# Optimization experiments

Hardware: AMD Instinct MI355X
Metric: run time of the kernel (lower is better)

Reference implementation:

```python
import jax, jax.numpy as jnp
import numpy as np

N = 20000      # nodes
E = 320000     # edges per relation
D = 128        # d_model
H = 2          # attention heads


def _gat(x, src, dst, W, al, ar, b):
    """DGL-style GATConv on a single relation (same src/dst node type).
    x: [N, in], W: [in, H*O], al/ar: [H, O], b: [H*O]. Returns [N, H, O]."""
    h, o = al.shape
    feat = (x @ W).reshape(N, h, o)                 # [N, H, O]
    el = jnp.sum(feat * al, axis=-1)                # [N, H]
    er = jnp.sum(feat * ar, axis=-1)                # [N, H]
    e = jax.nn.leaky_relu(el[src] + er[dst], 0.2)   # [E, H] per-edge logits
    m = jax.ops.segment_max(e, dst, num_segments=N)            # per-dst max
    ee = jnp.exp(e - m[dst])
    s = jax.ops.segment_sum(ee, dst, num_segments=N)
    alpha = ee / jnp.maximum(s[dst], 1e-9)          # edge softmax over incoming edges
    out = jax.ops.segment_sum(alpha[:, :, None] * feat[src], dst, num_segments=N)
    return out + b.reshape(1, h, o)


def setup_inputs() -> dict:
    key = jax.random.key(0)
    ks = jax.random.split(key, 24)
    d = {
        'x': jax.random.normal(ks[0], (N, D), jnp.float32),
        'src0': jax.random.randint(ks[1], (E,), 0, N, jnp.int32),
        'dst0': jax.random.randint(ks[2], (E,), 0, N, jnp.int32),
        'src1': jax.random.randint(ks[3], (E,), 0, N, jnp.int32),
        'dst1': jax.random.randint(ks[4], (E,), 0, N, jnp.int32),
    }
    sc = 0.1
    # layer 1: in=D, out per head=2D, heads=H
    d['W1_0'] = jax.random.normal(ks[5], (D, H * 2 * D), jnp.float32) * sc
    d['al1_0'] = jax.random.normal(ks[6], (H, 2 * D), jnp.float32) * sc
    d['ar1_0'] = jax.random.normal(ks[7], (H, 2 * D), jnp.float32) * sc
    d['b1_0'] = jnp.zeros((H * 2 * D,), jnp.float32)
    d['W1_1'] = jax.random.normal(ks[8], (D, H * 2 * D), jnp.float32) * sc
    d['al1_1'] = jax.random.normal(ks[9], (H, 2 * D), jnp.float32) * sc
    d['ar1_1'] = jax.random.normal(ks[10], (H, 2 * D), jnp.float32) * sc
    d['b1_1'] = jnp.zeros((H * 2 * D,), jnp.float32)
    # layer 2: in=2D, out per head=D, heads=H
    d['W2_0'] = jax.random.normal(ks[11], (2 * D, H * D), jnp.float32) * sc
    d['al2_0'] = jax.random.normal(ks[12], (H, D), jnp.float32) * sc
    d['ar2_0'] = jax.random.normal(ks[13], (H, D), jnp.float32) * sc
    d['b2_0'] = jnp.zeros((H * D,), jnp.float32)
    d['W2_1'] = jax.random.normal(ks[14], (2 * D, H * D), jnp.float32) * sc
    d['al2_1'] = jax.random.normal(ks[15], (H, D), jnp.float32) * sc
    d['ar2_1'] = jax.random.normal(ks[16], (H, D), jnp.float32) * sc
    d['b2_1'] = jnp.zeros((H * D,), jnp.float32)
    return d


def reference(x, src0, dst0, src1, dst1,
              W1_0, al1_0, ar1_0, b1_0, W1_1, al1_1, ar1_1, b1_1,
              W2_0, al2_0, ar2_0, b2_0, W2_1, al2_1, ar2_1, b2_1):
    # conv1: HeteroGraphConv sum over relations, then mean over heads, relu
    h1 = _gat(x, src0, dst0, W1_0, al1_0, ar1_0, b1_0) \
       + _gat(x, src1, dst1, W1_1, al1_1, ar1_1, b1_1)   # [N, H, 2D]
    h1 = jax.nn.relu(h1.mean(axis=1))                    # [N, 2D]; dropout is eval-mode identity
    # conv2: same structure, then mean over heads
    h2 = _gat(h1, src0, dst0, W2_0, al2_0, ar2_0, b2_0) \
       + _gat(h1, src1, dst1, W2_1, al2_1, ar2_1, b2_1)  # [N, H, D]
    return h2.mean(axis=1)                                # [N, D]
```

## Files before the change

kernel.cpp:

```cpp
#include <hip/hip_runtime.h>


#define NN 20000
#define NE 320000
#define LOG2E 1.44269504f

typedef unsigned short bf16_t;
typedef __attribute__((ext_vector_type(8))) short short8;
typedef __attribute__((ext_vector_type(4))) float f32x4;

__device__ __forceinline__ float bf2f(bf16_t u) {
    return __uint_as_float(((unsigned)u) << 16);
}
__device__ __forceinline__ bf16_t f2bf(float f) {
    unsigned x = __float_as_uint(f);
    unsigned r = (x + 0x7fffu + ((x >> 16) & 1u)) >> 16;
    return (bf16_t)r;
}
__device__ __forceinline__ unsigned pk2bf(float a, float b) {
    return (unsigned)f2bf(a) | ((unsigned)f2bf(b) << 16);
}
__device__ __forceinline__ float lrelu(float v) {
    return (v > 0.f) ? v : 0.2f * v;
}
__device__ __forceinline__ void load_x2(const void* x, int flag, int idx,
                                        float& v0, float& v1) {
    if (flag) {
        float2 f = ((const float2*)x)[idx];
        v0 = f.x; v1 = f.y;
    } else {
        unsigned pk = ((const unsigned*)x)[idx];
        v0 = bf2f((bf16_t)(pk & 0xffffu));
        v1 = bf2f((bf16_t)(pk >> 16));
    }
}

#define NTC 16
struct CzArgs {
    const void* src[NTC];
    bf16_t* dst[NTC];
    int n[NTC];
    int nblk[NTC + 1];
    int* zero_ptr;
    int zn;
    const unsigned* xsrc;
    int* flag_out;
};
__global__ void convzero_kernel(CzArgs a) {
    __shared__ int fl_s;
    int t = threadIdx.x;
    if (t < 64) {
        float mx = 0.f;
        for (int i = t; i < 256; i += 64) {
            float v = fabsf(bf2f((bf16_t)(a.xsrc[i] & 0xffffu)));
            v = (v <= 1e30f) ? v : 1e30f;
            mx = fmaxf(mx, v);
        }
        for (int off = 32; off > 0; off >>= 1) mx = fmaxf(mx, __shfl_xor(mx, off));
        if (t == 0) {
            int f = (mx > 1e6f) ? 1 : 0;
            fl_s = f;
            if (blockIdx.x == 0) *a.flag_out = f;
        }
    }
    __syncthreads();
    int flag = fl_s;
    int b = blockIdx.x;
    int ti = 0;
#pragma unroll 1
    for (; ti <= NTC; ++ti) {
        if (b < a.nblk[ti]) break;
        b -= a.nblk[ti];
    }
    int i = b * 256 + t;
    if (ti < NTC) {
        if (i < a.n[ti]) {
            if (flag) a.dst[ti][i] = f2bf(((const float*)a.src[ti])[i]);
            else      a.dst[ti][i] = ((const bf16_t*)a.src[ti])[i];
        }
    } else {
        if (i < a.zn) a.zero_ptr[i] = 0;
    }
}

struct PrepArgs {
    const bf16_t *W1[2], *W2[2];
    const bf16_t *al1[2], *ar1[2], *al2[2], *ar2[2];
    const bf16_t *b1[2], *b2[2];
    float *wal1, *war1;
    float *wal2, *war2;
    float *bc1, *bc2;
    bf16_t *Wc1f;
    bf16_t *Wzf;
};
__device__ __forceinline__ void prep_body(const PrepArgs& p, int bx, int tid) {
    if (bx < 4) {
        int t = bx * 256 + tid;
        int lr = t >> 9, rel = (t >> 8) & 1, h = (t >> 7) & 1, k = t & 127;
        const bf16_t* av = lr ? p.ar1[rel] : p.al1[rel];
        const bf16_t* W = p.W1[rel];
        float s = 0.f;
        for (int o = 0; o < 256; ++o)
            s += bf2f(W[k * 512 + h * 256 + o]) * bf2f(av[h * 256 + o]);
        (lr ? p.war1 : p.wal1)[(rel * 2 + h) * 128 + k] = s * LOG2E;
    } else if (bx < 12) {
        int t = (bx - 4) * 256 + tid;
        int lr = t >> 10, rel = (t >> 9) & 1, h = (t >> 8) & 1, k = t & 255;
        const bf16_t* av = lr ? p.ar2[rel] : p.al2[rel];
        const bf16_t* W = p.W2[rel];
        float s = 0.f;
        for (int o = 0; o < 128; ++o)
            s += bf2f(W[k * 256 + h * 128 + o]) * bf2f(av[h * 128 + o]);
        (lr ? p.war2 : p.wal2)[(rel * 2 + h) * 256 + k] = s * LOG2E;
    } else if (bx < 14) {
        int t = (bx - 12) * 256 + tid;
        if (t < 256) {
            p.bc1[t] = 0.5f * (bf2f(p.b1[0][t]) + bf2f(p.b1[0][256 + t]) +
                               bf2f(p.b1[1][t]) + bf2f(p.b1[1][256 + t]));
        } else if (t < 384) {
            int o = t - 256;
            p.bc2[o] = 0.5f * (bf2f(p.b2[0][o]) + bf2f(p.b2[0][128 + o]) +
                               bf2f(p.b2[1][o]) + bf2f(p.b2[1][128 + o]));
        }
    } else if (bx < 78) {
        int i = (bx - 14) * 256 + tid;
        int lane = i & 63;
        int t2 = i >> 6;
        int ct = t2 >> 4, ks = t2 & 15;
        int col = ct * 16 + (lane & 15);
        bf16_t* out = p.Wc1f + (size_t)i * 8;
#pragma unroll
        for (int j = 0; j < 8; ++j) {
            int r = ks * 32 + ((lane >> 4) << 3) + j;
            int rel = r >> 8, h = (r >> 7) & 1, kx = r & 127;
            out[j] = f2bf(0.5f * bf2f(p.W1[rel][kx * 512 + h * 256 + col]));
        }
    } else {
        int b = bx - 78;
        int rel = b >> 5;
        int i = (b & 31) * 256 + tid;
        int lane = i & 63;
        int t2 = i >> 6;
        int ct = t2 >> 3, ks = t2 & 7;
        int col = ct * 16 + (lane & 15);
        bf16_t* out = p.Wzf + (size_t)rel * 65536 + (size_t)i * 8;
#pragma unroll
        for (int j = 0; j < 8; ++j) {
            int r = ks * 32 + ((lane >> 4) << 3) + j;
            out[j] = f2bf(0.5f * bf2f(p.W2[rel][r * 256 + col]));
        }
    }
}

struct Csr2 {
    const int* src[2];
    const int* dst[2];
    int* cnt[2];
    int* offs[2];
    int* rank[2];
    int* srcc[2];
};
struct PhArgs { PrepArgs p; Csr2 c; };
__global__ void prep_hist_kernel(PhArgs a) {
    int bx = blockIdx.x;
    if (bx < 142) {
        prep_body(a.p, bx, threadIdx.x);
    } else {
        int b = bx - 142;
        int rel = b / 1250;
        int i = (b - rel * 1250) * 256 + threadIdx.x;
        if (i < NE)
            a.c.rank[rel][i] = atomicAdd(&a.c.cnt[rel][a.c.dst[rel][i]], 1);
    }
}

__global__ void scan2_kernel(Csr2 c, int n) {
    int rel = blockIdx.x;
    const int* cnt = c.cnt[rel];
    int* offs = c.offs[rel];
    __shared__ int sums[1024];
    int t = threadIdx.x;
    int chunk = (n + 1023) >> 10;
    int lo = t * chunk;
    int hi = min(lo + chunk, n);
    int s = 0;
    for (int i = lo; i < hi; ++i) s += cnt[i];
    sums[t] = s;
    __syncthreads();
    for (int off = 1; off < 1024; off <<= 1) {
        int v = (t >= off) ? sums[t - off] : 0;
        __syncthreads();
        sums[t] += v;
        __syncthreads();
    }
    int run = (t == 0) ? 0 : sums[t - 1];
    for (int i = lo; i < hi; ++i) { int v = cnt[i]; offs[i] = run; run += v; }
    if (t == 1023) offs[n] = sums[1023];
}

__global__ void scat_elr_kernel(Csr2 c, const void* __restrict__ x,
                                const int* __restrict__ flagp,
                                const float* __restrict__ wal1,
                                const float* __restrict__ war1,
                                float* __restrict__ el0, float* __restrict__ er0,
                                float* __restrict__ el1, float* __restrict__ er1) {
    __shared__ float wl[512], wr[512];
    int t = threadIdx.x;
    if (blockIdx.x < 5000) {
        wl[t] = wal1[t]; wl[t + 256] = wal1[t + 256];
        wr[t] = war1[t]; wr[t + 256] = war1[t + 256];
        __syncthreads();
        int fl = *flagp;
        int w = t >> 6, lane = t & 63;
        int node = blockIdx.x * 4 + w;
        float v0, v1;
        load_x2(x, fl, node * 64 + lane, v0, v1);
        float de[4], dr[4];
#pragma unroll
        for (int cch = 0; cch < 4; ++cch) {
            de[cch] = v0 * wl[cch * 128 + 2 * lane] + v1 * wl[cch * 128 + 2 * lane + 1];
            dr[cch] = v0 * wr[cch * 128 + 2 * lane] + v1 * wr[cch * 128 + 2 * lane + 1];
        }
#pragma unroll
        for (int off = 32; off > 0; off >>= 1) {
#pragma unroll
            for (int cch = 0; cch < 4; ++cch) {
                de[cch] += __shfl_xor(de[cch], off);
                dr[cch] += __shfl_xor(dr[cch], off);
            }
        }
        if (lane == 0) {
            el0[node * 2 + 0] = de[0]; el0[node * 2 + 1] = de[1];
            el1[node * 2 + 0] = de[2]; el1[node * 2 + 1] = de[3];
            er0[node * 2 + 0] = dr[0]; er0[node * 2 + 1] = dr[1];
            er1[node * 2 + 0] = dr[2]; er1[node * 2 + 1] = dr[3];
        }
    } else {
        int b = blockIdx.x - 5000;
        int rel = b / 313;
        int base = (b - rel * 313) * 1024 + t * 4;
        const int* dstp = c.dst[rel];
        const int* srcp = c.src[rel];
        const int* rkp  = c.rank[rel];
        const int* offp = c.offs[rel];
        int* sc = c.srcc[rel];
        if (base + 3 < NE) {
            int4 dv = *(const int4*)(dstp + base);
            int4 rv = *(const int4*)(rkp + base);
            int4 sv = *(const int4*)(srcp + base);
            sc[offp[dv.x] + rv.x] = sv.x;
            sc[offp[dv.y] + rv.y] = sv.y;
            sc[offp[dv.z] + rv.z] = sv.z;
            sc[offp[dv.w] + rv.w] = sv.w;
        } else {
            for (int k = 0; k < 4 && base + k < NE; ++k)
                sc[offp[dstp[base + k]] + rkp[base + k]] = srcp[base + k];
        }
    }
}

__device__ __forceinline__ void wave_softmax(
    const int* __restrict__ srcc, int beg, int deg,
    const float* __restrict__ el, float er_h0, float er_h1, int lane,
    int& sreg, float& a0, float& a1,
    float& m0, float& i0, float& m1, float& i1) {
    float mm0 = -1e30f, ss0 = 0.f, mm1 = -1e30f, ss1 = 0.f;
    float e0r = 0.f, e1r = 0.f;
    sreg = 0;
    for (int j = lane; j < deg; j += 64) {
        int s = srcc[beg + j];
        float2 ev = ((const float2*)el)[s];
        float e0 = lrelu(ev.x + er_h0);
        float e1 = lrelu(ev.y + er_h1);
        if (j < 64) { sreg = s; e0r = e0; e1r = e1; }
        float mn0 = fmaxf(mm0, e0);
        ss0 = ss0 * exp2f(mm0 - mn0) + exp2f(e0 - mn0);
        mm0 = mn0;
        float mn1 = fmaxf(mm1, e1);
        ss1 = ss1 * exp2f(mm1 - mn1) + exp2f(e1 - mn1);
        mm1 = mn1;
    }
#pragma unroll
    for (int off = 1; off < 64; off <<= 1) {
        float om = __shfl_xor(mm0, off), os = __shfl_xor(ss0, off);
        float mn = fmaxf(mm0, om);
        ss0 = ss0 * exp2f(mm0 - mn) + os * exp2f(om - mn);
        mm0 = mn;
        om = __shfl_xor(mm1, off); os = __shfl_xor(ss1, off);
        mn = fmaxf(mm1, om);
        ss1 = ss1 * exp2f(mm1 - mn) + os * exp2f(om - mn);
        mm1 = mn;
    }
    m0 = mm0; m1 = mm1;
    i0 = 1.f / fmaxf(ss0, 1e-9f);
    i1 = 1.f / fmaxf(ss1, 1e-9f);
    a0 = exp2f(e0r - m0) * i0;
    a1 = exp2f(e1r - m1) * i1;
}

__global__ void agg1_kernel(
    const int* __restrict__ offs0, const int* __restrict__ srcc0,
    const float* __restrict__ el0, const float* __restrict__ er0,
    const int* __restrict__ offs1, const int* __restrict__ srcc1,
    const float* __restrict__ el1, const float* __restrict__ er1,
    const void* __restrict__ x, const int* __restrict__ flagp,
    bf16_t* __restrict__ y1) {
    int t = threadIdx.x;
    int w = t >> 6, lane = t & 63;
    int slot = lane >> 5, m = lane & 31;
    int d = blockIdx.x * 2 + (w >> 1);
    int rel = w & 1;
    const int* offs = rel ? offs1 : offs0;
    const int* srcc = rel ? srcc1 : srcc0;
    const float* el = rel ? el1 : el0;
    const float* er = rel ? er1 : er0;
    int beg = offs[d], deg = offs[d + 1] - beg;
    float erh0 = er[d * 2], erh1 = er[d * 2 + 1];
    int fl = *flagp;

    int sr;
    float a0, a1, m0, i0, m1, i1;
    wave_softmax(srcc, beg, deg, el, erh0, erh1, lane, sr, a0, a1, m0, i0, m1, i1);

    auto xload = [&](int s, float v[4]) {
        if (fl) {
            float4 f = ((const float4*)x)[s * 32 + m];
            v[0] = f.x; v[1] = f.y; v[2] = f.z; v[3] = f.w;
        } else {
            uint2 pk = ((const uint2*)x)[s * 32 + m];
            v[0] = bf2f((bf16_t)(pk.x & 0xffffu));
            v[1] = bf2f((bf16_t)(pk.x >> 16));
            v[2] = bf2f((bf16_t)(pk.y & 0xffffu));
            v[3] = bf2f((bf16_t)(pk.y >> 16));
        }
    };
    float h0[4] = {}, h1[4] = {};
    {
        int dm = min(deg, 64);
        int T = (dm + 3) & ~3;
        for (int jj = slot; jj < T; jj += 4) {
            int j2 = jj + 2;
            int sA = __shfl(sr, jj), sB = __shfl(sr, j2);
            float pA0 = __shfl(a0, jj), pA1 = __shfl(a1, jj);
            float pB0 = __shfl(a0, j2), pB1 = __shfl(a1, j2);
            if (jj >= dm) { sA = 0; pA0 = 0.f; pA1 = 0.f; }
            if (j2 >= dm) { sB = 0; pB0 = 0.f; pB1 = 0.f; }
            float vA[4], vB[4];
            xload(sA, vA);
            xload(sB, vB);
#pragma unroll
            for (int k = 0; k < 4; ++k) {
                h0[k] += pA0 * vA[k] + pB0 * vB[k];
                h1[k] += pA1 * vA[k] + pB1 * vB[k];
            }
        }
        for (int jj = 64 + slot; jj < deg; jj += 2) {
            int sA = srcc[beg + jj];
            float2 ev = ((const float2*)el)[sA];
            float pA0 = exp2f(lrelu(ev.x + erh0) - m0) * i0;
            float pA1 = exp2f(lrelu(ev.y + erh1) - m1) * i1;
            float vA[4];
            xload(sA, vA);
#pragma unroll
            for (int k = 0; k < 4; ++k) {
                h0[k] += pA0 * vA[k];
                h1[k] += pA1 * vA[k];
            }
        }
    }
#pragma unroll
    for (int k = 0; k < 4; ++k) {
        h0[k] += __shfl_xor(h0[k], 32);
        h1[k] += __shfl_xor(h1[k], 32);
    }
    if (slot == 0) {
        bf16_t* yr = y1 + (size_t)d * 512 + rel * 256;
        uint2 u;
        u.x = pk2bf(h0[0], h0[1]); u.y = pk2bf(h0[2], h0[3]);
        ((uint2*)yr)[m] = u;
        u.x = pk2bf(h1[0], h1[1]); u.y = pk2bf(h1[2], h1[3]);
        ((uint2*)(yr + 128))[m] = u;
    }
}

__global__ void gemm1_kernel(const bf16_t* __restrict__ A, const bf16_t* __restrict__ Wf,
                             const float* __restrict__ bc1, bf16_t* __restrict__ h1,
                             const float* __restrict__ wal2, const float* __restrict__ war2,
                             float* __restrict__ el2_0, float* __restrict__ er2_0,
                             float* __restrict__ el2_1, float* __restrict__ er2_1,
                             int n) {
    constexpr int K = 512, M = 256, KS = 16, NF = 8;
    int w = threadIdx.x >> 6, lane = threadIdx.x & 63;
    int q = lane >> 4, m16 = lane & 15;
    int rf = blockIdx.y * 64 + w * 16;
    if (rf >= n) return;
    f32x4 acc[NF] = {};
    const bf16_t* Arow = A + (size_t)(rf + m16) * K + q * 8;
    for (int ks = 0; ks < KS; ++ks) {
        short8 af = *(const short8*)(Arow + ks * 32);
#pragma unroll
        for (int f = 0; f < NF; ++f) {
            int ct = blockIdx.x * NF + f;
            short8 bfr = *(const short8*)(Wf + ((size_t)(ct * KS + ks) * 64 + lane) * 8);
            acc[f] = __builtin_amdgcn_mfma_f32_16x16x32_bf16(af, bfr, acc[f], 0, 0, 0);
        }
    }
    int col0 = blockIdx.x * (NF * 16);
    float del[2][2][4] = {};
    float der[2][2][4] = {};
#pragma unroll
    for (int f = 0; f < NF; ++f) {
        int col = col0 + f * 16 + m16;
        float bcv = bc1[col];
        float wle[2][2], wre[2][2];
#pragma unroll
        for (int rel = 0; rel < 2; ++rel)
#pragma unroll
            for (int h = 0; h < 2; ++h) {
                wle[rel][h] = wal2[(rel * 2 + h) * 256 + col];
                wre[rel][h] = war2[(rel * 2 + h) * 256 + col];
            }
#pragma unroll
        for (int r = 0; r < 4; ++r) {
            int row = rf + q * 4 + r;
            float v = fmaxf(acc[f][r] + bcv, 0.f);
            bf16_t hb = f2bf(v);
            h1[(size_t)row * M + col] = hb;
            float vb = bf2f(hb);
#pragma unroll
            for (int rel = 0; rel < 2; ++rel)
#pragma unroll
                for (int h = 0; h < 2; ++h) {
                    del[rel][h][r] += vb * wle[rel][h];
                    der[rel][h][r] += vb * wre[rel][h];
                }
        }
    }
#pragma unroll
    for (int off = 1; off < 16; off <<= 1) {
#pragma unroll
        for (int rel = 0; rel < 2; ++rel)
#pragma unroll
            for (int h = 0; h < 2; ++h)
#pragma unroll
                for (int r = 0; r < 4; ++r) {
                    del[rel][h][r] += __shfl_xor(del[rel][h][r], off);
                    der[rel][h][r] += __shfl_xor(der[rel][h][r], off);
                }
    }
    if (m16 == 0) {
#pragma unroll
        for (int r = 0; r < 4; ++r) {
            int row = rf + q * 4 + r;
            atomicAdd(&el2_0[row * 2 + 0], del[0][0][r]);
            atomicAdd(&el2_0[row * 2 + 1], del[0][1][r]);
            atomicAdd(&el2_1[row * 2 + 0], del[1][0][r]);
            atomicAdd(&el2_1[row * 2 + 1], del[1][1][r]);
            atomicAdd(&er2_0[row * 2 + 0], der[0][0][r]);
            atomicAdd(&er2_0[row * 2 + 1], der[0][1][r]);
            atomicAdd(&er2_1[row * 2 + 0], der[1][0][r]);
            atomicAdd(&er2_1[row * 2 + 1], der[1][1][r]);
        }
    }
}

__global__ void gemmz_kernel(const bf16_t* __restrict__ A, const bf16_t* __restrict__ Wzf,
                             bf16_t* __restrict__ z, int n) {
    constexpr int K = 256, M = 256, KS = 8, NF = 8;
    int rel = blockIdx.z;
    const bf16_t* Wf = Wzf + (size_t)rel * 65536;
    bf16_t* C = z + (size_t)rel * NN * 256;
    int w = threadIdx.x >> 6, lane = threadIdx.x & 63;
    int q = lane >> 4, m16 = lane & 15;
    int rf = blockIdx.y * 64 + w * 16;
    if (rf >= n) return;
    f32x4 acc[NF] = {};
    const bf16_t* Arow = A + (size_t)(rf + m16) * K + q * 8;
    for (int ks = 0; ks < KS; ++ks) {
        short8 af = *(const short8*)(Arow + ks * 32);
#pragma unroll
        for (int f = 0; f < NF; ++f) {
            int ct = blockIdx.x * NF + f;
            short8 bfr = *(const short8*)(Wf + ((size_t)(ct * KS + ks) * 64 + lane) * 8);
            acc[f] = __builtin_amdgcn_mfma_f32_16x16x32_bf16(af, bfr, acc[f], 0, 0, 0);
        }
    }
    int col0 = blockIdx.x * (NF * 16);
#pragma unroll
    for (int f = 0; f < NF; ++f) {
#pragma unroll
        for (int r = 0; r < 4; ++r) {
            int row = rf + q * 4 + r;
            C[(size_t)row * M + col0 + f * 16 + m16] = f2bf(acc[f][r]);
        }
    }
}

__global__ void aggout_kernel(
    const int* __restrict__ offs0, const int* __restrict__ srcc0,
    const float* __restrict__ el0, const float* __restrict__ er0,
    const int* __restrict__ offs1, const int* __restrict__ srcc1,
    const float* __restrict__ el1, const float* __restrict__ er1,
    const bf16_t* __restrict__ z, const float* __restrict__ bc2,
    void* __restrict__ out, const int* __restrict__ flagp) {
    __shared__ float sh[4][128];
    int t = threadIdx.x;
    int w = t >> 6, lane = t & 63;
    int slot = lane >> 5, m = lane & 31;
    int h = m >> 4;
    int d = blockIdx.x * 2 + (w >> 1);
    int rel = w & 1;
    const int* offs = rel ? offs1 : offs0;
    const int* srcc = rel ? srcc1 : srcc0;
    const float* el = rel ? el1 : el0;
    const float* er = rel ? er1 : er0;
    int beg = offs[d], deg = offs[d + 1] - beg;
    float erh0 = er[d * 2], erh1 = er[d * 2 + 1];

    int sr;
    float a0, a1, m0, i0, m1, i1;
    wave_softmax(srcc, beg, deg, el, erh0, erh1, lane, sr, a0, a1, m0, i0, m1, i1);

    float acc[8] = {};
    auto fmadd8 = [&](float a, uint4 p) {
        acc[0] += a * bf2f((bf16_t)(p.x & 0xffffu));
        acc[1] += a * bf2f((bf16_t)(p.x >> 16));
        acc[2] += a * bf2f((bf16_t)(p.y & 0xffffu));
        acc[3] += a * bf2f((bf16_t)(p.y >> 16));
        acc[4] += a * bf2f((bf16_t)(p.z & 0xffffu));
        acc[5] += a * bf2f((bf16_t)(p.z >> 16));
        acc[6] += a * bf2f((bf16_t)(p.w & 0xffffu));
        acc[7] += a * bf2f((bf16_t)(p.w >> 16));
    };
    {
        const uint4* zp = (const uint4*)(z + (size_t)rel * NN * 256);
        int dm = min(deg, 64);
        int T = (dm + 3) & ~3;
        for (int jj = slot; jj < T; jj += 4) {
            int j2 = jj + 2;
            int sA = __shfl(sr, jj), sB = __shfl(sr, j2);
            float xA0 = __shfl(a0, jj), xA1 = __shfl(a1, jj);
            float xB0 = __shfl(a0, j2), xB1 = __shfl(a1, j2);
            float aA = h ? xA1 : xA0;
            float aB = h ? xB1 : xB0;
            if (jj >= dm) { sA = 0; aA = 0.f; }
            if (j2 >= dm) { sB = 0; aB = 0.f; }
            uint4 pA = zp[sA * 32 + m];
            uint4 pB = zp[sB * 32 + m];
            fmadd8(aA, pA);
            fmadd8(aB, pB);
        }
        for (int jj = 64 + slot; jj < deg; jj += 2) {
            int sA = srcc[beg + jj];
            float2 ev = ((const float2*)el)[sA];
            float aA = h ? (exp2f(lrelu(ev.y + erh1) - m1) * i1)
                         : (exp2f(lrelu(ev.x + erh0) - m0) * i0);
            uint4 pA = zp[sA * 32 + m];
            fmadd8(aA, pA);
        }
    }
#pragma unroll
    for (int k = 0; k < 8; ++k) acc[k] += __shfl_xor(acc[k], 32);
#pragma unroll
    for (int k = 0; k < 8; ++k) acc[k] += __shfl_xor(acc[k], 16);
    if (slot == 0 && m < 16) {
#pragma unroll
        for (int k = 0; k < 8; ++k) sh[w][m * 8 + k] = acc[k];
    }
    __syncthreads();
    int ni = t >> 7;
    int o = t & 127;
    int dd = blockIdx.x * 2 + ni;
    float v = bc2[o] + sh[ni * 2][o] + sh[ni * 2 + 1][o];
    if (*flagp) ((float*)out)[(size_t)dd * 128 + o] = v;
    else        ((bf16_t*)out)[(size_t)dd * 128 + o] = f2bf(v);
}

extern "C" void kernel_launch(void* const* d_in, const int* in_sizes, int n_in,
                              void* d_out, int out_size, void* d_ws, size_t ws_size,
                              hipStream_t stream) {
    (void)in_sizes; (void)n_in; (void)out_size; (void)ws_size;
    const void* x0 = d_in[0];
    const int* src0 = (const int*)d_in[1];
    const int* dst0 = (const int*)d_in[2];
    const int* src1 = (const int*)d_in[3];
    const int* dst1 = (const int*)d_in[4];

    char* ws = (char*)d_ws;
    size_t off = 0;
    auto alloc = [&](size_t bytes) -> void* {
        void* p = ws + off;
        off = (off + bytes + 255) & ~(size_t)255;
        return p;
    };
    int* flag = (int*)alloc(4);
    static const int tn[NTC] = {128 * 512, 512, 512, 512,
                                128 * 512, 512, 512, 512,
                                256 * 256, 256, 256, 256,
                                256 * 256, 256, 256, 256};
    bf16_t* tb[NTC];
    for (int i = 0; i < NTC; ++i) tb[i] = (bf16_t*)alloc((size_t)tn[i] * 2);

    bf16_t* Wc1f = (bf16_t*)alloc((size_t)512 * 256 * 2);
    bf16_t* Wzf  = (bf16_t*)alloc((size_t)2 * 65536 * 2);
    float* wal1 = (float*)alloc(512 * 4);
    float* war1 = (float*)alloc(512 * 4);
    float* wal2 = (float*)alloc(1024 * 4);
    float* war2 = (float*)alloc(1024 * 4);
    float* bc1  = (float*)alloc(256 * 4);
    float* bc2  = (float*)alloc(128 * 4);

    char* zbeg = ws + off;
    int* cnt0 = (int*)alloc(NN * 4);
    int* cnt1 = (int*)alloc(NN * 4);
    float* el2_0 = (float*)alloc(NN * 2 * 4);
    float* er2_0 = (float*)alloc(NN * 2 * 4);
    float* el2_1 = (float*)alloc(NN * 2 * 4);
    float* er2_1 = (float*)alloc(NN * 2 * 4);
    char* zend = ws + off;
    int zcount = (int)((zend - zbeg) >> 2);

    int* offs0 = (int*)alloc((NN + 1) * 4);
    int* offs1 = (int*)alloc((NN + 1) * 4);
    int* rank0 = (int*)alloc(NE * 4);
    int* rank1 = (int*)alloc(NE * 4);
    int* srcc0 = (int*)alloc(NE * 4);
    int* srcc1 = (int*)alloc(NE * 4);
    float* el1_0 = (float*)alloc(NN * 2 * 4);
    float* er1_0 = (float*)alloc(NN * 2 * 4);
    float* el1_1 = (float*)alloc(NN * 2 * 4);
    float* er1_1 = (float*)alloc(NN * 2 * 4);
    bf16_t* h1 = (bf16_t*)alloc((size_t)NN * 256 * 2);
    bf16_t* Y  = (bf16_t*)alloc((size_t)NN * 1024 * 2);
    bf16_t* y1 = Y;
    bf16_t* z  = Y;

    CzArgs cz;
    static const int din_idx[NTC] = {5, 6, 7, 8, 9, 10, 11, 12,
                                     13, 14, 15, 16, 17, 18, 19, 20};
    int total_blocks = 0;
    for (int i = 0; i < NTC; ++i) {
        cz.src[i] = d_in[din_idx[i]];
        cz.dst[i] = tb[i];
        cz.n[i] = tn[i];
        cz.nblk[i] = (tn[i] + 255) / 256;
        total_blocks += cz.nblk[i];
    }
    cz.zero_ptr = (int*)zbeg;
    cz.zn = zcount;
    cz.nblk[NTC] = (zcount + 255) / 256;
    total_blocks += cz.nblk[NTC];
    cz.xsrc = (const unsigned*)x0;
    cz.flag_out = flag;
    convzero_kernel<<<total_blocks, 256, 0, stream>>>(cz);

    PhArgs ph;
    ph.p.W1[0] = tb[0];  ph.p.W1[1] = tb[4];
    ph.p.W2[0] = tb[8];  ph.p.W2[1] = tb[12];
    ph.p.al1[0] = tb[1]; ph.p.ar1[0] = tb[2];
    ph.p.al1[1] = tb[5]; ph.p.ar1[1] = tb[6];
    ph.p.al2[0] = tb[9]; ph.p.ar2[0] = tb[10];
    ph.p.al2[1] = tb[13]; ph.p.ar2[1] = tb[14];
    ph.p.b1[0] = tb[3];  ph.p.b1[1] = tb[7];
    ph.p.b2[0] = tb[11]; ph.p.b2[1] = tb[15];
    ph.p.wal1 = wal1; ph.p.war1 = war1;
    ph.p.wal2 = wal2; ph.p.war2 = war2;
    ph.p.bc1 = bc1; ph.p.bc2 = bc2;
    ph.p.Wc1f = Wc1f; ph.p.Wzf = Wzf;
    ph.c.src[0] = src0; ph.c.src[1] = src1;
    ph.c.dst[0] = dst0; ph.c.dst[1] = dst1;
    ph.c.cnt[0] = cnt0; ph.c.cnt[1] = cnt1;
    ph.c.offs[0] = offs0; ph.c.offs[1] = offs1;
    ph.c.rank[0] = rank0; ph.c.rank[1] = rank1;
    ph.c.srcc[0] = srcc0; ph.c.srcc[1] = srcc1;
    prep_hist_kernel<<<142 + 2500, 256, 0, stream>>>(ph);

    scan2_kernel<<<2, 1024, 0, stream>>>(ph.c, NN);

    scat_elr_kernel<<<5000 + 626, 256, 0, stream>>>(
        ph.c, x0, flag, wal1, war1, el1_0, er1_0, el1_1, er1_1);

    agg1_kernel<<<10000, 256, 0, stream>>>(offs0, srcc0, el1_0, er1_0,
                                           offs1, srcc1, el1_1, er1_1, x0, flag, y1);

    gemm1_kernel<<<dim3(2, 313), 256, 0, stream>>>(
        y1, Wc1f, bc1, h1, wal2, war2, el2_0, er2_0, el2_1, er2_1, NN);

    gemmz_kernel<<<dim3(2, 313, 2), 256, 0, stream>>>(h1, Wzf, z, NN);

    aggout_kernel<<<10000, 256, 0, stream>>>(offs0, srcc0, el2_0, er2_0,
                                             offs1, srcc1, el2_1, er2_1,
                                             z, bc2, d_out, flag);
}
```

Before: 315.6 us.

## Split CSR histogram into 8 sub-counters and trim softmax shuffle reduction

The per-destination degree histogram is now spread over 8 sub-arrays chosen by block index, so concurrent atomics on the same destination contend less. The scan sums the sub-counters and writes per-sub-bucket offsets, which the scatter uses so that the existing per-sub ranks stay valid. Separately, the wave softmax cross-lane reduction stops early once the offset reaches the power of two covering the active lane count, skipping shuffles for low-degree nodes. The cost is an 8x larger counter array to zero and scan, plus a serial 8-way inner loop in the single-block scan.

Result: slower. 448.0 us (+42.0%).

```diff
diff --git a/kernel.cpp b/kernel.cpp
--- a/kernel.cpp
+++ b/kernel.cpp
@@ -157,6 +157,7 @@
     const int* dst[2];
     int* cnt[2];
     int* offs[2];
+    int* osub[2];
     int* rank[2];
     int* srcc[2];
 };
@@ -168,9 +169,13 @@
     } else {
         int b = bx - 142;
         int rel = b / 1250;
-        int i = (b - rel * 1250) * 256 + threadIdx.x;
-        if (i < NE)
-            a.c.rank[rel][i] = atomicAdd(&a.c.cnt[rel][a.c.dst[rel][i]], 1);
+        int blkrel = b - rel * 1250;
+        int i = blkrel * 256 + threadIdx.x;
+        if (i < NE) {
+            int sub = blkrel & 7;
+            a.c.rank[rel][i] =
+                atomicAdd(&a.c.cnt[rel][sub * NN + a.c.dst[rel][i]], 1);
+        }
     }
 }
 
@@ -178,13 +183,17 @@
     int rel = blockIdx.x;
     const int* cnt = c.cnt[rel];
     int* offs = c.offs[rel];
+    int* osub = c.osub[rel];
     __shared__ int sums[1024];
     int t = threadIdx.x;
     int chunk = (n + 1023) >> 10;
     int lo = t * chunk;
     int hi = min(lo + chunk, n);
     int s = 0;
-    for (int i = lo; i < hi; ++i) s += cnt[i];
+    for (int i = lo; i < hi; ++i) {
+#pragma unroll
+        for (int k = 0; k < 8; ++k) s += cnt[k * n + i];
+    }
     sums[t] = s;
     __syncthreads();
     for (int off = 1; off < 1024; off <<= 1) {
@@ -194,7 +203,14 @@
         __syncthreads();
     }
     int run = (t == 0) ? 0 : sums[t - 1];
-    for (int i = lo; i < hi; ++i) { int v = cnt[i]; offs[i] = run; run += v; }
+    for (int i = lo; i < hi; ++i) {
+        offs[i] = run;
+#pragma unroll
+        for (int k = 0; k < 8; ++k) {
+            osub[k * n + i] = run;
+            run += cnt[k * n + i];
+        }
+    }
     if (t == 1023) offs[n] = sums[1023];
 }
 
@@ -242,19 +258,20 @@
         const int* dstp = c.dst[rel];
         const int* srcp = c.src[rel];
         const int* rkp  = c.rank[rel];
-        const int* offp = c.offs[rel];
+        int sub = (base >> 8) & 7;
+        const int* osub = c.osub[rel] + sub * NN;
         int* sc = c.srcc[rel];
         if (base + 3 < NE) {
             int4 dv = *(const int4*)(dstp + base);
             int4 rv = *(const int4*)(rkp + base);
             int4 sv = *(const int4*)(srcp + base);
-            sc[offp[dv.x] + rv.x] = sv.x;
-            sc[offp[dv.y] + rv.y] = sv.y;
-            sc[offp[dv.z] + rv.z] = sv.z;
-            sc[offp[dv.w] + rv.w] = sv.w;
+            sc[osub[dv.x] + rv.x] = sv.x;
+            sc[osub[dv.y] + rv.y] = sv.y;
+            sc[osub[dv.z] + rv.z] = sv.z;
+            sc[osub[dv.w] + rv.w] = sv.w;
         } else {
             for (int k = 0; k < 4 && base + k < NE; ++k)
-                sc[offp[dstp[base + k]] + rkp[base + k]] = srcp[base + k];
+                sc[osub[dstp[base + k]] + rkp[base + k]] = srcp[base + k];
         }
     }
 }
@@ -280,8 +297,11 @@
         ss1 = ss1 * exp2f(mm1 - mn1) + exp2f(e1 - mn1);
         mm1 = mn1;
     }
+    int dc = min(deg, 64);
+    int dpow = (dc <= 1) ? dc : (1 << (32 - __clz(dc - 1)));
 #pragma unroll
     for (int off = 1; off < 64; off <<= 1) {
+        if (off >= dpow) break;
         float om = __shfl_xor(mm0, off), os = __shfl_xor(ss0, off);
         float mn = fmaxf(mm0, om);
         ss0 = ss0 * exp2f(mm0 - mn) + os * exp2f(om - mn);
@@ -611,8 +631,8 @@
     float* bc2  = (float*)alloc(128 * 4);
 
     char* zbeg = ws + off;
-    int* cnt0 = (int*)alloc(NN * 4);
-    int* cnt1 = (int*)alloc(NN * 4);
+    int* cnt0 = (int*)alloc((size_t)8 * NN * 4);
+    int* cnt1 = (int*)alloc((size_t)8 * NN * 4);
     float* el2_0 = (float*)alloc(NN * 2 * 4);
     float* er2_0 = (float*)alloc(NN * 2 * 4);
     float* el2_1 = (float*)alloc(NN * 2 * 4);
@@ -622,6 +642,8 @@
 
     int* offs0 = (int*)alloc((NN + 1) * 4);
     int* offs1 = (int*)alloc((NN + 1) * 4);
+    int* osub0 = (int*)alloc((size_t)8 * NN * 4);
+    int* osub1 = (int*)alloc((size_t)8 * NN * 4);
     int* rank0 = (int*)alloc(NE * 4);
     int* rank1 = (int*)alloc(NE * 4);
     int* srcc0 = (int*)alloc(NE * 4);
@@ -671,6 +693,7 @@
     ph.c.dst[0] = dst0; ph.c.dst[1] = dst1;
     ph.c.cnt[0] = cnt0; ph.c.cnt[1] = cnt1;
     ph.c.offs[0] = offs0; ph.c.offs[1] = offs1;
+    ph.c.osub[0] = osub0; ph.c.osub[1] = osub1;
     ph.c.rank[0] = rank0; ph.c.rank[1] = rank1;
     ph.c.srcc[0] = srcc0; ph.c.srcc[1] = srcc1;
     prep_hist_kernel<<<142 + 2500, 256, 0, stream>>>(ph);
```

## Replace two-block CSR offset scan with three-phase multi-block scan; trim softmax shuffles

Applied to the files above, without the earlier changes.

The serial-chunk scan, which ran in only two 1024-thread blocks each walking about 20 elements, is replaced by a block-local scan over 79 blocks per relation, a small top-level scan of block sums, and a fix-up kernel that writes the offsets. This spreads the prefix sum over many CUs to cut its latency. The cost is two extra launches and extra scratch buffers. Separately, the wave-level max/sum reduction in the edge-softmax now stops early when a node has fewer than 64 incoming edges, skipping shuffle steps that would only combine empty lanes.

New measurement: 297.9 us. -5.6%, faster.

```diff
diff --git a/kernel.cpp b/kernel.cpp
--- a/kernel.cpp
+++ b/kernel.cpp
@@ -4,6 +4,7 @@
 #define NN 20000
 #define NE 320000
 #define LOG2E 1.44269504f
+#define NB 79
 
 typedef unsigned short bf16_t;
 typedef __attribute__((ext_vector_type(8))) short short8;
@@ -159,6 +160,8 @@
     int* offs[2];
     int* rank[2];
     int* srcc[2];
+    int* npfx[2];
+    int* bsum[2];
 };
 struct PhArgs { PrepArgs p; Csr2 c; };
 __global__ void prep_hist_kernel(PhArgs a) {
@@ -174,28 +177,46 @@
     }
 }
 
-__global__ void scan2_kernel(Csr2 c, int n) {
+__global__ void scan_blk_kernel(Csr2 c) {
+    int rel = blockIdx.y;
+    int t = threadIdx.x;
+    int i = blockIdx.x * 256 + t;
+    int tot = (i < NN) ? c.cnt[rel][i] : 0;
+    __shared__ int sh[256];
+    sh[t] = tot;
+    __syncthreads();
+    for (int off = 1; off < 256; off <<= 1) {
+        int v = (t >= off) ? sh[t - off] : 0;
+        __syncthreads();
+        sh[t] += v;
+        __syncthreads();
+    }
+    if (i < NN) c.npfx[rel][i] = sh[t] - tot;
+    if (t == 255) c.bsum[rel][blockIdx.x] = sh[255];
+}
+
+__global__ void scan_top_kernel(Csr2 c) {
     int rel = blockIdx.x;
-    const int* cnt = c.cnt[rel];
-    int* offs = c.offs[rel];
-    __shared__ int sums[1024];
     int t = threadIdx.x;
-    int chunk = (n + 1023) >> 10;
-    int lo = t * chunk;
-    int hi = min(lo + chunk, n);
-    int s = 0;
-    for (int i = lo; i < hi; ++i) s += cnt[i];
-    sums[t] = s;
+    __shared__ int sh[128];
+    int v = (t < NB) ? c.bsum[rel][t] : 0;
+    sh[t] = v;
     __syncthreads();
-    for (int off = 1; off < 1024; off <<= 1) {
-        int v = (t >= off) ? sums[t - off] : 0;
+    for (int off = 1; off < 128; off <<= 1) {
+        int u = (t >= off) ? sh[t - off] : 0;
         __syncthreads();
-        sums[t] += v;
+        sh[t] += u;
         __syncthreads();
     }
-    int run = (t == 0) ? 0 : sums[t - 1];
-    for (int i = lo; i < hi; ++i) { int v = cnt[i]; offs[i] = run; run += v; }
-    if (t == 1023) offs[n] = sums[1023];
+    if (t < NB) c.bsum[rel][t] = sh[t] - v;
+    if (t == 0) c.offs[rel][NN] = NE;
+}
+
+__global__ void scan_fin_kernel(Csr2 c) {
+    int rel = blockIdx.y;
+    int i = blockIdx.x * 256 + threadIdx.x;
+    if (i < NN)
+        c.offs[rel][i] = c.bsum[rel][blockIdx.x] + c.npfx[rel][i];
 }
 
 __global__ void scat_elr_kernel(Csr2 c, const void* __restrict__ x,
@@ -280,8 +301,11 @@
         ss1 = ss1 * exp2f(mm1 - mn1) + exp2f(e1 - mn1);
         mm1 = mn1;
     }
+    int dc = min(deg, 64);
+    int dpow = (dc <= 1) ? dc : (1 << (32 - __clz(dc - 1)));
 #pragma unroll
     for (int off = 1; off < 64; off <<= 1) {
+        if (off >= dpow) break;
         float om = __shfl_xor(mm0, off), os = __shfl_xor(ss0, off);
         float mn = fmaxf(mm0, om);
         ss0 = ss0 * exp2f(mm0 - mn) + os * exp2f(om - mn);
@@ -622,6 +646,10 @@
 
     int* offs0 = (int*)alloc((NN + 1) * 4);
     int* offs1 = (int*)alloc((NN + 1) * 4);
+    int* npfx0 = (int*)alloc(NN * 4);
+    int* npfx1 = (int*)alloc(NN * 4);
+    int* bsum0 = (int*)alloc(128 * 4);
+    int* bsum1 = (int*)alloc(128 * 4);
     int* rank0 = (int*)alloc(NE * 4);
     int* rank1 = (int*)alloc(NE * 4);
     int* srcc0 = (int*)alloc(NE * 4);
@@ -673,9 +701,13 @@
     ph.c.offs[0] = offs0; ph.c.offs[1] = offs1;
     ph.c.rank[0] = rank0; ph.c.rank[1] = rank1;
     ph.c.srcc[0] = srcc0; ph.c.srcc[1] = srcc1;
+    ph.c.npfx[0] = npfx0; ph.c.npfx[1] = npfx1;
+    ph.c.bsum[0] = bsum0; ph.c.bsum[1] = bsum1;
     prep_hist_kernel<<<142 + 2500, 256, 0, stream>>>(ph);
 
-    scan2_kernel<<<2, 1024, 0, stream>>>(ph.c, NN);
+    scan_blk_kernel<<<dim3(NB, 2), 256, 0, stream>>>(ph.c);
+    scan_top_kernel<<<2, 128, 0, stream>>>(ph.c);
+    scan_fin_kernel<<<dim3(NB, 2), 256, 0, stream>>>(ph.c);
 
     scat_elr_kernel<<<5000 + 626, 256, 0, stream>>>(
         ph.c, x0, flag, wal1, war1, el1_0, er1_0, el1_1, er1_1);
```
